# Performance work log

Measured on AMD Instinct MI355X. Metric: run time of the kernel, lower is better.

The kernel has to match this reference:

```python
import jax, jax.numpy as jnp
import numpy as np

DIMS = (2000, 500, 400)
H, DK, DV = 8, 32, 32
DM = H * DV  # 256
NUM_CLASS = 5
BS = 16384
TEMP = DK ** 0.5
LN_EPS = 1e-6


def setup_inputs() -> dict:
    key = jax.random.key(0)
    ks = jax.random.split(key, 32)
    inp = {"input_data": jax.random.normal(ks[0], (BS, sum(DIMS)), dtype=jnp.float32)}
    i = 1
    for name, odim in (("q", H * DK), ("k", H * DK), ("v", H * DV)):
        for m, d in enumerate(DIMS):
            inp[f"w{name}{m}"] = jax.random.normal(ks[i], (d, odim), dtype=jnp.float32) * (1.0 / np.sqrt(d)); i += 1
            inp[f"b{name}{m}"] = jnp.zeros((odim,), dtype=jnp.float32)
    inp["fc_w"] = jax.random.normal(ks[i], (DM, DM), dtype=jnp.float32) * (1.0 / np.sqrt(DM)); i += 1
    inp["fc_b"] = jnp.zeros((DM,), dtype=jnp.float32)
    inp["ln_g"] = jnp.ones((DM,), dtype=jnp.float32)
    inp["ln_b"] = jnp.zeros((DM,), dtype=jnp.float32)
    inp["out_w"] = jax.random.normal(ks[i], (len(DIMS) * DM, NUM_CLASS), dtype=jnp.float32) * (1.0 / np.sqrt(len(DIMS) * DM)); i += 1
    inp["out_b"] = jnp.zeros((NUM_CLASS,), dtype=jnp.float32)
    return inp


def _forward(input_data, wq, bq, wk, bk, wv, bv, fc_w, fc_b, ln_g, ln_b, out_w, out_b):
    bs = input_data.shape[0]
    M = len(DIMS)
    offs = np.concatenate([[0], np.cumsum(DIMS)])
    xs = [input_data[:, offs[m]:offs[m + 1]] for m in range(M)]
    # per-modality projections -> [bs, M, H*D]
    q = jnp.stack([xs[m] @ wq[m] + bq[m] for m in range(M)], axis=1)
    k = jnp.stack([xs[m] @ wk[m] + bk[m] for m in range(M)], axis=1)
    v = jnp.stack([xs[m] @ wv[m] + bv[m] for m in range(M)], axis=1)
    # [bs, H, M, D]
    qh = q.reshape(bs, M, H, DK).transpose(0, 2, 1, 3)
    kh = k.reshape(bs, M, H, DK).transpose(0, 2, 1, 3)
    vh = v.reshape(bs, M, H, DV).transpose(0, 2, 1, 3)
    attn = jnp.einsum("bhmd,bhnd->bhmn", qh / TEMP, kh)
    attn = attn / jnp.abs(attn.min())  # global-min scaling as in source
    attn = attn / jnp.maximum(jnp.sum(jnp.abs(attn), axis=-1, keepdims=True), 1e-12)  # L1 normalize
    attn = jax.nn.softmax(attn, axis=-1)
    o = jnp.einsum("bhmn,bhnd->bhmd", attn, vh)
    o = o.transpose(0, 2, 1, 3).reshape(bs, M, DM)
    residual = v  # [bs, M, DM]
    o = o @ fc_w + fc_b
    x = o + residual
    mu = x.mean(axis=-1, keepdims=True)
    var = ((x - mu) ** 2).mean(axis=-1, keepdims=True)
    x = (x - mu) / jnp.sqrt(var + LN_EPS) * ln_g + ln_b
    return x.reshape(bs, -1) @ out_w + out_b


def reference(input_data, wq0, bq0, wq1, bq1, wq2, bq2, wk0, bk0, wk1, bk1, wk2, bk2,
              wv0, bv0, wv1, bv1, wv2, bv2, fc_w, fc_b, ln_g, ln_b, out_w, out_b):
    return _forward(input_data, (wq0, wq1, wq2), (bq0, bq1, bq2), (wk0, wk1, wk2), (bk0, bk1, bk2),
                    (wv0, wv1, wv2), (bv0, bv1, bv2), fc_w, fc_b, ln_g, ln_b, out_w, out_b)
```

## Files before the change

### kernel.cpp

```cpp
#include <hip/hip_runtime.h>
#include <hip/hip_bf16.h>

#define BATCH 16384
#define HEADS 8
#define DDK 32
#define NQKV 768
#define NCLASS 5
#define LN_EPS 1e-6f

#define BM 128
#define BN 128
#define BKK 32

typedef _Float16 f16x8 __attribute__((ext_vector_type(8)));
typedef float f32x4 __attribute__((ext_vector_type(4)));

__device__ __forceinline__ void gl16(const void* g, void* l) {
    __builtin_amdgcn_global_load_lds(
        (const __attribute__((address_space(1))) unsigned int*)g,
        (__attribute__((address_space(3))) unsigned int*)l, 16, 0, 0);
}

__global__ __launch_bounds__(256) void convert_x(const float* __restrict__ X,
                                                 _Float16* __restrict__ A,
                                                 int Kdim, int Kpad, int xoff,
                                                 int r0, int nrows) {
    const int k8n = Kpad >> 3;
    const int total = nrows * k8n;
    for (int i = blockIdx.x * blockDim.x + threadIdx.x; i < total;
         i += gridDim.x * blockDim.x) {
        const int rl = i / k8n;
        const int k8 = (i - rl * k8n) << 3;
        const float* src = X + (size_t)(r0 + rl) * 2900 + xoff + k8;
        float xv[8];
        if (k8 + 8 <= Kdim) {
            float4 v0 = *reinterpret_cast<const float4*>(src);
            float4 v1 = *reinterpret_cast<const float4*>(src + 4);
            xv[0] = v0.x; xv[1] = v0.y; xv[2] = v0.z; xv[3] = v0.w;
            xv[4] = v1.x; xv[5] = v1.y; xv[6] = v1.z; xv[7] = v1.w;
        } else {
#pragma unroll
            for (int j = 0; j < 8; ++j) xv[j] = (k8 + j < Kdim) ? src[j] : 0.f;
        }
        union { _Float16 h[8]; uint4 v; } hi, lo;
#pragma unroll
        for (int j = 0; j < 8; ++j) {
            hi.h[j] = (_Float16)xv[j];
            lo.h[j] = (_Float16)(xv[j] - (float)hi.h[j]);
        }
        _Float16* dst = A + (size_t)rl * (2 * Kpad) + k8;
        *reinterpret_cast<uint4*>(dst) = hi.v;
        *reinterpret_cast<uint4*>(dst + Kpad) = lo.v;
    }
}

struct WArgs {
    const float* w[3][3];
    const float* b[3][3];
    const float* fcw;
    _Float16* Bt;
    float* biasx;
    _Float16* fcWh;
};

__global__ __launch_bounds__(256) void convert_w_all(WArgs a) {
    const int y = blockIdx.y;
    const int gid = blockIdx.x * 256 + threadIdx.x;
    if (y < 3) {
        const int m = y;
        const int Kdim = (m == 0) ? 2000 : (m == 1 ? 500 : 400);
        const int Kpad = (m == 0) ? 2048 : (m == 1 ? 512 : 448);
        if (gid < NQKV) {
            const int p = gid >> 8, c = gid & 255;
            a.biasx[m * NQKV + gid] = a.b[p][m][c];
        }
        const int k8n = Kpad >> 3;
        const int total = NQKV * k8n;
        _Float16* dst0 = a.Bt + (size_t)m * NQKV * 2048;
        for (int i = gid; i < total; i += gridDim.x * 256) {
            const int kb = i / NQKV;
            const int n = i - kb * NQKV;
            const int k8 = kb << 3;
            const int p = n >> 8, c = n & 255;
            const float* wsrc = a.w[p][m];
            union { _Float16 h[8]; uint4 v; } hi;
#pragma unroll
            for (int j = 0; j < 8; ++j) {
                float x = (k8 + j < Kdim) ? wsrc[(size_t)(k8 + j) * 256 + c] : 0.f;
                hi.h[j] = (_Float16)x;
            }
            *reinterpret_cast<uint4*>(dst0 + (size_t)n * Kpad + k8) = hi.v;
        }
    } else {
        for (int i = gid; i < 256 * 32; i += gridDim.x * 256) {
            const int n = i & 255;
            const int k8 = (i >> 8) << 3;
            union { _Float16 h[8]; uint4 v; } hi;
#pragma unroll
            for (int j = 0; j < 8; ++j)
                hi.h[j] = (_Float16)a.fcw[(size_t)(k8 + j) * 256 + n];
            *reinterpret_cast<uint4*>(a.fcWh + (size_t)n * 256 + k8) = hi.v;
        }
    }
}

__global__ __launch_bounds__(256) void qkv_mfma(
    const _Float16* __restrict__ A,
    const _Float16* __restrict__ Bt,
    const float* __restrict__ bias,
    float* __restrict__ Qo, float* __restrict__ Ko, float* __restrict__ Vo,
    int Kpad, int mz, int r0) {
    const int ld = 2 * Kpad;
    const int row0l = blockIdx.x * BM;
    const int nb = blockIdx.y * BN;
    const int tid = threadIdx.x;
    const int lane = tid & 63;
    const int w = tid >> 6;
    const int wr = w >> 1, wc = w & 1;

    __shared__ alignas(16) _Float16 AsH[BM * BKK];
    __shared__ alignas(16) _Float16 AsL[BM * BKK];
    __shared__ alignas(16) _Float16 BsH[BN * BKK];

    f32x4 acc[4][4];
#pragma unroll
    for (int i = 0; i < 4; ++i)
#pragma unroll
        for (int j = 0; j < 4; ++j) acc[i][j] = (f32x4){0.f, 0.f, 0.f, 0.f};

    const int rs = lane >> 2;
    const int kk = (lane & 3) * 8;
    const size_t gA0 = (size_t)(row0l + w * 16 + rs) * ld + kk;
    const size_t gA1 = (size_t)(row0l + (w + 4) * 16 + rs) * ld + kk;
    const size_t gB0 = (size_t)(nb + w * 16 + rs) * Kpad + kk;
    const size_t gB1 = (size_t)(nb + (w + 4) * 16 + rs) * Kpad + kk;
    _Float16* lAH0 = &AsH[w * 512];
    _Float16* lAH1 = &AsH[(w + 4) * 512];
    _Float16* lAL0 = &AsL[w * 512];
    _Float16* lAL1 = &AsL[(w + 4) * 512];
    _Float16* lBH0 = &BsH[w * 512];
    _Float16* lBH1 = &BsH[(w + 4) * 512];

    const int fr = lane & 15;
    const int fk = (lane >> 4) * 8;
    const int aoff0 = (wr * 64 + fr) * BKK + fk;
    const int boff0 = (wc * 64 + fr) * BKK + fk;

    const int nk = Kpad >> 5;
#pragma unroll 1
    for (int kt = 0; kt < nk; ++kt) {
        const int k0 = kt * BKK;
        __syncthreads();
        gl16(A + gA0 + k0, lAH0);
        gl16(A + gA1 + k0, lAH1);
        gl16(A + Kpad + gA0 + k0, lAL0);
        gl16(A + Kpad + gA1 + k0, lAL1);
        gl16(Bt + gB0 + k0, lBH0);
        gl16(Bt + gB1 + k0, lBH1);
        __syncthreads();

        f16x8 ah[4], bh[4];
#pragma unroll
        for (int mi = 0; mi < 4; ++mi)
            ah[mi] = *reinterpret_cast<const f16x8*>(&AsH[aoff0 + mi * 16 * BKK]);
#pragma unroll
        for (int ni = 0; ni < 4; ++ni)
            bh[ni] = *reinterpret_cast<const f16x8*>(&BsH[boff0 + ni * 16 * BKK]);
#pragma unroll
        for (int mi = 0; mi < 4; ++mi)
#pragma unroll
            for (int ni = 0; ni < 4; ++ni)
                acc[mi][ni] = __builtin_amdgcn_mfma_f32_16x16x32_f16(
                    ah[mi], bh[ni], acc[mi][ni], 0, 0, 0);
        {
            f16x8 al[4];
#pragma unroll
            for (int mi = 0; mi < 4; ++mi)
                al[mi] = *reinterpret_cast<const f16x8*>(&AsL[aoff0 + mi * 16 * BKK]);
#pragma unroll
            for (int mi = 0; mi < 4; ++mi)
#pragma unroll
                for (int ni = 0; ni < 4; ++ni)
                    acc[mi][ni] = __builtin_amdgcn_mfma_f32_16x16x32_f16(
                        al[mi], bh[ni], acc[mi][ni], 0, 0, 0);
        }
    }

#pragma unroll
    for (int ni = 0; ni < 4; ++ni) {
        const int gc = nb + wc * 64 + ni * 16 + fr;
        const int proj = gc >> 8;
        const int col = gc & 255;
        const float bv = bias[gc];
        float* outp = (proj == 0 ? Qo : proj == 1 ? Ko : Vo);
#pragma unroll
        for (int mi = 0; mi < 4; ++mi) {
            const int gr = r0 + row0l + wr * 64 + mi * 16 + (lane >> 4) * 4;
            float* p = outp + (size_t)gr * NQKV + mz * 256 + col;
#pragma unroll
            for (int j = 0; j < 4; ++j)
                p[(size_t)j * NQKV] = acc[mi][ni][j] + bv;
        }
    }
}

__global__ __launch_bounds__(256) void attn_kernel(const float* __restrict__ Q,
                                                   const float* __restrict__ K,
                                                   const float* __restrict__ V,
                                                   _Float16* __restrict__ Of) {
    const int s = blockIdx.x;
    const int t = threadIdx.x;
    __shared__ float qs[NQKV], ks[NQKV], vs[NQKV];
    __shared__ float att[HEADS][3][3];

    const size_t base = (size_t)s * NQKV;
    for (int i = t; i < NQKV; i += 256) {
        qs[i] = Q[base + i];
        ks[i] = K[base + i];
        vs[i] = V[base + i];
    }
    __syncthreads();

    if (t < 72) {
        const int h = t / 9, ij = t % 9, i = ij / 3, j = ij % 3;
        const float* qp = &qs[i * 256 + h * 32];
        const float* kp = &ks[j * 256 + h * 32];
        float sc = 0.f;
#pragma unroll
        for (int d = 0; d < DDK; ++d) sc = fmaf(qp[d], kp[d], sc);
        att[h][i][j] = sc;
    }
    __syncthreads();
    if (t < 24) {
        const int h = t / 3, i = t % 3;
        float s0 = att[h][i][0], s1 = att[h][i][1], s2 = att[h][i][2];
        float r = fabsf(s0) + fabsf(s1) + fabsf(s2);
        r = fmaxf(r, 1e-12f);
        float p0 = s0 / r, p1 = s1 / r, p2 = s2 / r;
        float mx = fmaxf(p0, fmaxf(p1, p2));
        float e0 = expf(p0 - mx), e1 = expf(p1 - mx), e2 = expf(p2 - mx);
        float inv = 1.f / (e0 + e1 + e2);
        att[h][i][0] = e0 * inv;
        att[h][i][1] = e1 * inv;
        att[h][i][2] = e2 * inv;
    }
    __syncthreads();

    const int c = t;
    const int h = c >> 5;
#pragma unroll
    for (int m = 0; m < 3; ++m) {
        float o = att[h][m][0] * vs[c] + att[h][m][1] * vs[256 + c] + att[h][m][2] * vs[512 + c];
        const size_t ob = ((size_t)s * 3 + m) * 512 + c;
        _Float16 oh = (_Float16)o;
        Of[ob] = oh;
        Of[ob + 256] = (_Float16)(o - (float)oh);
    }
}

__global__ __launch_bounds__(256) void fc_mfma(const _Float16* __restrict__ O,
                                               const _Float16* __restrict__ Wh,
                                               const float* __restrict__ fcb,
                                               const float* __restrict__ resid,
                                               float* __restrict__ X) {
    const int row0 = blockIdx.x * BM;
    const int nb = blockIdx.y * BN;
    const int tid = threadIdx.x;
    const int lane = tid & 63;
    const int w = tid >> 6;
    const int wr = w >> 1, wc = w & 1;

    __shared__ alignas(16) _Float16 AsH[BM * BKK];
    __shared__ alignas(16) _Float16 AsL[BM * BKK];
    __shared__ alignas(16) _Float16 BsH[BN * BKK];

    f32x4 acc[4][4];
#pragma unroll
    for (int i = 0; i < 4; ++i)
#pragma unroll
        for (int j = 0; j < 4; ++j) acc[i][j] = (f32x4){0.f, 0.f, 0.f, 0.f};

    const int rs = lane >> 2;
    const int kk = (lane & 3) * 8;
    const size_t gA0 = (size_t)(row0 + w * 16 + rs) * 512 + kk;
    const size_t gA1 = (size_t)(row0 + (w + 4) * 16 + rs) * 512 + kk;
    const size_t gB0 = (size_t)(nb + w * 16 + rs) * 256 + kk;
    const size_t gB1 = (size_t)(nb + (w + 4) * 16 + rs) * 256 + kk;
    _Float16* lAH0 = &AsH[w * 512];
    _Float16* lAH1 = &AsH[(w + 4) * 512];
    _Float16* lAL0 = &AsL[w * 512];
    _Float16* lAL1 = &AsL[(w + 4) * 512];
    _Float16* lBH0 = &BsH[w * 512];
    _Float16* lBH1 = &BsH[(w + 4) * 512];

    const int fr = lane & 15;
    const int fk = (lane >> 4) * 8;
    const int aoff0 = (wr * 64 + fr) * BKK + fk;
    const int boff0 = (wc * 64 + fr) * BKK + fk;

#pragma unroll 1
    for (int kt = 0; kt < 8; ++kt) {
        const int k0 = kt * BKK;
        __syncthreads();
        gl16(O + gA0 + k0, lAH0);
        gl16(O + gA1 + k0, lAH1);
        gl16(O + 256 + gA0 + k0, lAL0);
        gl16(O + 256 + gA1 + k0, lAL1);
        gl16(Wh + gB0 + k0, lBH0);
        gl16(Wh + gB1 + k0, lBH1);
        __syncthreads();

        f16x8 ah[4], bh[4];
#pragma unroll
        for (int mi = 0; mi < 4; ++mi)
            ah[mi] = *reinterpret_cast<const f16x8*>(&AsH[aoff0 + mi * 16 * BKK]);
#pragma unroll
        for (int ni = 0; ni < 4; ++ni)
            bh[ni] = *reinterpret_cast<const f16x8*>(&BsH[boff0 + ni * 16 * BKK]);
#pragma unroll
        for (int mi = 0; mi < 4; ++mi)
#pragma unroll
            for (int ni = 0; ni < 4; ++ni)
                acc[mi][ni] = __builtin_amdgcn_mfma_f32_16x16x32_f16(
                    ah[mi], bh[ni], acc[mi][ni], 0, 0, 0);
        {
            f16x8 al[4];
#pragma unroll
            for (int mi = 0; mi < 4; ++mi)
                al[mi] = *reinterpret_cast<const f16x8*>(&AsL[aoff0 + mi * 16 * BKK]);
#pragma unroll
            for (int mi = 0; mi < 4; ++mi)
#pragma unroll
                for (int ni = 0; ni < 4; ++ni)
                    acc[mi][ni] = __builtin_amdgcn_mfma_f32_16x16x32_f16(
                        al[mi], bh[ni], acc[mi][ni], 0, 0, 0);
        }
    }

#pragma unroll
    for (int ni = 0; ni < 4; ++ni) {
        const int gc = nb + wc * 64 + ni * 16 + fr;
        const float bv = fcb[gc];
#pragma unroll
        for (int mi = 0; mi < 4; ++mi) {
            const int gr = row0 + wr * 64 + mi * 16 + (lane >> 4) * 4;
#pragma unroll
            for (int j = 0; j < 4; ++j) {
                const size_t off = (size_t)(gr + j) * 256 + gc;
                X[off] = acc[mi][ni][j] + bv + resid[off];
            }
        }
    }
}

__global__ __launch_bounds__(256) void ln_out_kernel(const float* __restrict__ X,
                                                     const float* __restrict__ g,
                                                     const float* __restrict__ bb,
                                                     const float* __restrict__ ow,
                                                     const float* __restrict__ ob,
                                                     float* __restrict__ out) {
    const int s = blockIdx.x;
    const int t = threadIdx.x;
    const int lane = t & 63, wv = t >> 6;
    __shared__ float xr[NQKV];
    __shared__ float red1[4], red2[4];
    __shared__ float cpart[4][NCLASS];

    const size_t base = (size_t)s * NQKV;
    const float gg = g[t];
    const float bbv = bb[t];

    for (int m = 0; m < 3; ++m) {
        float v = X[base + m * 256 + t];
        float s1 = v, s2 = v * v;
#pragma unroll
        for (int off = 32; off > 0; off >>= 1) {
            s1 += __shfl_down(s1, off);
            s2 += __shfl_down(s2, off);
        }
        if (lane == 0) { red1[wv] = s1; red2[wv] = s2; }
        __syncthreads();
        const float tot = red1[0] + red1[1] + red1[2] + red1[3];
        const float tot2 = red2[0] + red2[1] + red2[2] + red2[3];
        const float mu = tot * (1.f / 256.f);
        const float var = tot2 * (1.f / 256.f) - mu * mu;
        const float inv = 1.0f / sqrtf(var + LN_EPS);
        xr[m * 256 + t] = (v - mu) * inv * gg + bbv;
        __syncthreads();
    }

    float p[NCLASS] = {0.f, 0.f, 0.f, 0.f, 0.f};
    for (int i = t; i < NQKV; i += 256) {
        const float xv = xr[i];
#pragma unroll
        for (int c = 0; c < NCLASS; ++c) p[c] = fmaf(xv, ow[i * NCLASS + c], p[c]);
    }
#pragma unroll
    for (int c = 0; c < NCLASS; ++c) {
        float pv = p[c];
#pragma unroll
        for (int off = 32; off > 0; off >>= 1) pv += __shfl_down(pv, off);
        if (lane == 0) cpart[wv][c] = pv;
    }
    __syncthreads();
    if (t < NCLASS)
        out[(size_t)s * NCLASS + t] =
            cpart[0][t] + cpart[1][t] + cpart[2][t] + cpart[3][t] + ob[t];
}

extern "C" void kernel_launch(void* const* d_in, const int* in_sizes, int n_in,
                              void* d_out, int out_size, void* d_ws, size_t ws_size,
                              hipStream_t stream) {
    const float* x = (const float*)d_in[0];
    WArgs wa;
    int idx = 1;
    for (int p = 0; p < 3; ++p)
        for (int m = 0; m < 3; ++m) {
            wa.w[p][m] = (const float*)d_in[idx++];
            wa.b[p][m] = (const float*)d_in[idx++];
        }
    const float* fc_w = (const float*)d_in[19];
    const float* fc_b = (const float*)d_in[20];
    const float* ln_g = (const float*)d_in[21];
    const float* ln_b = (const float*)d_in[22];
    const float* out_w = (const float*)d_in[23];
    const float* out_b = (const float*)d_in[24];

    float* ws = (float*)d_ws;
    const size_t SZ = (size_t)BATCH * NQKV;
    float* Q = ws;
    float* Kb = ws + SZ;
    float* Vb = ws + 2 * SZ;
    float* biasx = ws + 3 * SZ;
    _Float16* Bt = (_Float16*)(biasx + 3 * NQKV);
    _Float16* fcWh = Bt + (size_t)3 * NQKV * 2048;
    _Float16* pool = fcWh + 256 * 256;

    wa.fcw = fc_w; wa.Bt = Bt; wa.biasx = biasx; wa.fcWh = fcWh;

    const size_t fixed_bytes = (size_t)((char*)pool - (char*)d_ws);
    const size_t avail = (ws_size > fixed_bytes) ? ws_size - fixed_bytes : 0;

    float* X = Q;
    _Float16* Of = pool;

    const int Kdim[3] = {2000, 500, 400};
    const int Kpad[3] = {2048, 512, 448};
    const int xoff[3] = {0, 2000, 2500};

    convert_w_all<<<dim3(768, 4), 256, 0, stream>>>(wa);

    for (int m = 0; m < 3; ++m) {
        size_t rc = (avail / ((size_t)4 * Kpad[m])) & ~(size_t)127;
        if (rc < 128) rc = 128;
        if (rc > BATCH) rc = BATCH;
        const int rows_chunk = (int)rc;
        for (int r0 = 0; r0 < BATCH; r0 += rows_chunk) {
            const int nr = (BATCH - r0 < rows_chunk) ? (BATCH - r0) : rows_chunk;
            const int cgrid = ((nr * (Kpad[m] >> 3)) + 255) / 256;
            convert_x<<<(cgrid < 2048 ? cgrid : 2048), 256, 0, stream>>>(
                x, pool, Kdim[m], Kpad[m], xoff[m], r0, nr);
            dim3 g(nr / BM, NQKV / BN);
            qkv_mfma<<<g, 256, 0, stream>>>(pool, Bt + (size_t)m * NQKV * 2048,
                                            biasx + m * NQKV, Q, Kb, Vb,
                                            Kpad[m], m, r0);
        }
    }

    attn_kernel<<<BATCH, 256, 0, stream>>>(Q, Kb, Vb, Of);

    fc_mfma<<<dim3((BATCH * 3) / BM, 2), 256, 0, stream>>>(Of, fcWh, fc_b, Vb, X);

    ln_out_kernel<<<BATCH, 256, 0, stream>>>(X, ln_g, ln_b, out_w, out_b, (float*)d_out);
}
```

Baseline: 733.7 us.

## Merge per-modality QKV GEMMs into one launch with concatenated hi/lo K

```diff
diff --git a/kernel.cpp b/kernel.cpp
--- a/kernel.cpp
+++ b/kernel.cpp
@@ -21,16 +21,28 @@
         (__attribute__((address_space(3))) unsigned int*)l, 16, 0, 0);
 }
 
-__global__ __launch_bounds__(256) void convert_x(const float* __restrict__ X,
-                                                 _Float16* __restrict__ A,
-                                                 int Kdim, int Kpad, int xoff,
-                                                 int r0, int nrows) {
-    const int k8n = Kpad >> 3;
-    const int total = nrows * k8n;
+__global__ __launch_bounds__(256) void convert_x_all(const float* __restrict__ X,
+                                                     _Float16* __restrict__ A0,
+                                                     _Float16* __restrict__ A1,
+                                                     _Float16* __restrict__ A2,
+                                                     int r0, int nrows) {
+    const int total = nrows * 384;
     for (int i = blockIdx.x * blockDim.x + threadIdx.x; i < total;
          i += gridDim.x * blockDim.x) {
-        const int rl = i / k8n;
-        const int k8 = (i - rl * k8n) << 3;
+        const int rl = i / 384;
+        const int slot = i - rl * 384;
+        int k8, Kdim, xoff, lo_off;
+        _Float16* dst;
+        if (slot < 256) {
+            k8 = slot << 3; Kdim = 2000; xoff = 0; lo_off = 2048;
+            dst = A0 + (size_t)rl * 4096 + k8;
+        } else if (slot < 320) {
+            k8 = (slot - 256) << 3; Kdim = 500; xoff = 2000; lo_off = 512;
+            dst = A1 + (size_t)rl * 1024 + k8;
+        } else {
+            k8 = (slot - 320) << 3; Kdim = 400; xoff = 2500; lo_off = 512;
+            dst = A2 + (size_t)rl * 1024 + k8;
+        }
         const float* src = X + (size_t)(r0 + rl) * 2900 + xoff + k8;
         float xv[8];
         if (k8 + 8 <= Kdim) {
@@ -48,9 +60,8 @@
             hi.h[j] = (_Float16)xv[j];
             lo.h[j] = (_Float16)(xv[j] - (float)hi.h[j]);
         }
-        _Float16* dst = A + (size_t)rl * (2 * Kpad) + k8;
         *reinterpret_cast<uint4*>(dst) = hi.v;
-        *reinterpret_cast<uint4*>(dst + Kpad) = lo.v;
+        *reinterpret_cast<uint4*>(dst + lo_off) = lo.v;
     }
 }
 
@@ -69,14 +80,17 @@
     if (y < 3) {
         const int m = y;
         const int Kdim = (m == 0) ? 2000 : (m == 1 ? 500 : 400);
-        const int Kpad = (m == 0) ? 2048 : (m == 1 ? 512 : 448);
+        const int Kpad = (m == 0) ? 2048 : 512;
         if (gid < NQKV) {
             const int p = gid >> 8, c = gid & 255;
             a.biasx[m * NQKV + gid] = a.b[p][m][c];
         }
+        _Float16* dst0 = a.Bt;
+        if (m >= 1) dst0 += (size_t)NQKV * 4096;
+        if (m == 2) dst0 += (size_t)NQKV * 1024;
+        const int ld = 2 * Kpad;
         const int k8n = Kpad >> 3;
         const int total = NQKV * k8n;
-        _Float16* dst0 = a.Bt + (size_t)m * NQKV * 2048;
         for (int i = gid; i < total; i += gridDim.x * 256) {
             const int kb = i / NQKV;
             const int n = i - kb * NQKV;
@@ -89,7 +103,8 @@
                 float x = (k8 + j < Kdim) ? wsrc[(size_t)(k8 + j) * 256 + c] : 0.f;
                 hi.h[j] = (_Float16)x;
             }
-            *reinterpret_cast<uint4*>(dst0 + (size_t)n * Kpad + k8) = hi.v;
+            *reinterpret_cast<uint4*>(dst0 + (size_t)n * ld + k8) = hi.v;
+            *reinterpret_cast<uint4*>(dst0 + (size_t)n * ld + Kpad + k8) = hi.v;
         }
     } else {
         for (int i = gid; i < 256 * 32; i += gridDim.x * 256) {
@@ -104,13 +119,23 @@
     }
 }
 
-__global__ __launch_bounds__(256) void qkv_mfma(
-    const _Float16* __restrict__ A,
-    const _Float16* __restrict__ Bt,
-    const float* __restrict__ bias,
+struct GemmArgs {
+    const _Float16* A[3];
+    const _Float16* B[3];
+    int keff[3];
+};
+
+__global__ __launch_bounds__(256) void qkv_mfma_all(
+    GemmArgs ga, const float* __restrict__ biasx,
     float* __restrict__ Qo, float* __restrict__ Ko, float* __restrict__ Vo,
-    int Kpad, int mz, int r0) {
-    const int ld = 2 * Kpad;
+    int r0) {
+    const int z = blockIdx.z;
+    const _Float16* __restrict__ A = ga.A[z];
+    const _Float16* __restrict__ Bt = ga.B[z];
+    const int ld = ga.keff[z];
+    const int nk = ld >> 5;
+    const float* __restrict__ bias = biasx + z * NQKV;
+
     const int row0l = blockIdx.x * BM;
     const int nb = blockIdx.y * BN;
     const int tid = threadIdx.x;
@@ -118,9 +143,8 @@
     const int w = tid >> 6;
     const int wr = w >> 1, wc = w & 1;
 
-    __shared__ alignas(16) _Float16 AsH[BM * BKK];
-    __shared__ alignas(16) _Float16 AsL[BM * BKK];
-    __shared__ alignas(16) _Float16 BsH[BN * BKK];
+    __shared__ alignas(16) _Float16 As[BM * BKK];
+    __shared__ alignas(16) _Float16 Bs[BN * BKK];
 
     f32x4 acc[4][4];
 #pragma unroll
@@ -131,59 +155,42 @@
     const int rs = lane >> 2;
     const int kk = (lane & 3) * 8;
     const size_t gA0 = (size_t)(row0l + w * 16 + rs) * ld + kk;
-    const size_t gA1 = (size_t)(row0l + (w + 4) * 16 + rs) * ld + kk;
-    const size_t gB0 = (size_t)(nb + w * 16 + rs) * Kpad + kk;
-    const size_t gB1 = (size_t)(nb + (w + 4) * 16 + rs) * Kpad + kk;
-    _Float16* lAH0 = &AsH[w * 512];
-    _Float16* lAH1 = &AsH[(w + 4) * 512];
-    _Float16* lAL0 = &AsL[w * 512];
-    _Float16* lAL1 = &AsL[(w + 4) * 512];
-    _Float16* lBH0 = &BsH[w * 512];
-    _Float16* lBH1 = &BsH[(w + 4) * 512];
+    const size_t gA1 = gA0 + (size_t)64 * ld;
+    const size_t gB0 = (size_t)(nb + w * 16 + rs) * ld + kk;
+    const size_t gB1 = gB0 + (size_t)64 * ld;
+    _Float16* lA0 = &As[(w * 16) * BKK];
+    _Float16* lA1 = &As[(64 + w * 16) * BKK];
+    _Float16* lB0 = &Bs[(w * 16) * BKK];
+    _Float16* lB1 = &Bs[(64 + w * 16) * BKK];
 
     const int fr = lane & 15;
     const int fk = (lane >> 4) * 8;
     const int aoff0 = (wr * 64 + fr) * BKK + fk;
     const int boff0 = (wc * 64 + fr) * BKK + fk;
 
-    const int nk = Kpad >> 5;
 #pragma unroll 1
     for (int kt = 0; kt < nk; ++kt) {
         const int k0 = kt * BKK;
         __syncthreads();
-        gl16(A + gA0 + k0, lAH0);
-        gl16(A + gA1 + k0, lAH1);
-        gl16(A + Kpad + gA0 + k0, lAL0);
-        gl16(A + Kpad + gA1 + k0, lAL1);
-        gl16(Bt + gB0 + k0, lBH0);
-        gl16(Bt + gB1 + k0, lBH1);
-        __syncthreads();
-
-        f16x8 ah[4], bh[4];
+        gl16(A + gA0 + k0, lA0);
+        gl16(A + gA1 + k0, lA1);
+        gl16(Bt + gB0 + k0, lB0);
+        gl16(Bt + gB1 + k0, lB1);
+        __syncthreads();
+
+        f16x8 a[4], b[4];
 #pragma unroll
         for (int mi = 0; mi < 4; ++mi)
-            ah[mi] = *reinterpret_cast<const f16x8*>(&AsH[aoff0 + mi * 16 * BKK]);
+            a[mi] = *reinterpret_cast<const f16x8*>(&As[aoff0 + mi * 16 * BKK]);
 #pragma unroll
         for (int ni = 0; ni < 4; ++ni)
-            bh[ni] = *reinterpret_cast<const f16x8*>(&BsH[boff0 + ni * 16 * BKK]);
+            b[ni] = *reinterpret_cast<const f16x8*>(&Bs[boff0 + ni * 16 * BKK]);
 #pragma unroll
         for (int mi = 0; mi < 4; ++mi)
 #pragma unroll
             for (int ni = 0; ni < 4; ++ni)
                 acc[mi][ni] = __builtin_amdgcn_mfma_f32_16x16x32_f16(
-                    ah[mi], bh[ni], acc[mi][ni], 0, 0, 0);
-        {
-            f16x8 al[4];
-#pragma unroll
-            for (int mi = 0; mi < 4; ++mi)
-                al[mi] = *reinterpret_cast<const f16x8*>(&AsL[aoff0 + mi * 16 * BKK]);
-#pragma unroll
-            for (int mi = 0; mi < 4; ++mi)
-#pragma unroll
-                for (int ni = 0; ni < 4; ++ni)
-                    acc[mi][ni] = __builtin_amdgcn_mfma_f32_16x16x32_f16(
-                        al[mi], bh[ni], acc[mi][ni], 0, 0, 0);
-        }
+                    a[mi], b[ni], acc[mi][ni], 0, 0, 0);
     }
 
 #pragma unroll
@@ -196,7 +203,7 @@
 #pragma unroll
         for (int mi = 0; mi < 4; ++mi) {
             const int gr = r0 + row0l + wr * 64 + mi * 16 + (lane >> 4) * 4;
-            float* p = outp + (size_t)gr * NQKV + mz * 256 + col;
+            float* p = outp + (size_t)gr * NQKV + z * 256 + col;
 #pragma unroll
             for (int j = 0; j < 4; ++j)
                 p[(size_t)j * NQKV] = acc[mi][ni][j] + bv;
@@ -433,38 +440,41 @@
     float* Vb = ws + 2 * SZ;
     float* biasx = ws + 3 * SZ;
     _Float16* Bt = (_Float16*)(biasx + 3 * NQKV);
-    _Float16* fcWh = Bt + (size_t)3 * NQKV * 2048;
+    _Float16* fcWh = Bt + (size_t)NQKV * 6144;
     _Float16* pool = fcWh + 256 * 256;
 
     wa.fcw = fc_w; wa.Bt = Bt; wa.biasx = biasx; wa.fcWh = fcWh;
 
     const size_t fixed_bytes = (size_t)((char*)pool - (char*)d_ws);
     const size_t avail = (ws_size > fixed_bytes) ? ws_size - fixed_bytes : 0;
+    size_t rc = (avail / 12288) & ~(size_t)127;
+    if (rc < 128) rc = 128;
+    if (rc > BATCH) rc = BATCH;
+    const int rows_chunk = (int)rc;
 
     float* X = Q;
     _Float16* Of = pool;
 
-    const int Kdim[3] = {2000, 500, 400};
-    const int Kpad[3] = {2048, 512, 448};
-    const int xoff[3] = {0, 2000, 2500};
-
     convert_w_all<<<dim3(768, 4), 256, 0, stream>>>(wa);
 
-    for (int m = 0; m < 3; ++m) {
-        size_t rc = (avail / ((size_t)4 * Kpad[m])) & ~(size_t)127;
-        if (rc < 128) rc = 128;
-        if (rc > BATCH) rc = BATCH;
-        const int rows_chunk = (int)rc;
-        for (int r0 = 0; r0 < BATCH; r0 += rows_chunk) {
-            const int nr = (BATCH - r0 < rows_chunk) ? (BATCH - r0) : rows_chunk;
-            const int cgrid = ((nr * (Kpad[m] >> 3)) + 255) / 256;
-            convert_x<<<(cgrid < 2048 ? cgrid : 2048), 256, 0, stream>>>(
-                x, pool, Kdim[m], Kpad[m], xoff[m], r0, nr);
-            dim3 g(nr / BM, NQKV / BN);
-            qkv_mfma<<<g, 256, 0, stream>>>(pool, Bt + (size_t)m * NQKV * 2048,
-                                            biasx + m * NQKV, Q, Kb, Vb,
-                                            Kpad[m], m, r0);
-        }
+    GemmArgs ga;
+    ga.keff[0] = 4096; ga.keff[1] = 1024; ga.keff[2] = 1024;
+    ga.B[0] = Bt;
+    ga.B[1] = Bt + (size_t)NQKV * 4096;
+    ga.B[2] = Bt + (size_t)NQKV * 5120;
+
+    _Float16* A0 = pool;
+    _Float16* A1 = A0 + (size_t)rows_chunk * 4096;
+    _Float16* A2 = A1 + (size_t)rows_chunk * 1024;
+    ga.A[0] = A0; ga.A[1] = A1; ga.A[2] = A2;
+
+    for (int r0 = 0; r0 < BATCH; r0 += rows_chunk) {
+        const int nr = (BATCH - r0 < rows_chunk) ? (BATCH - r0) : rows_chunk;
+        const int cgrid = (nr * 384 + 255) / 256;
+        convert_x_all<<<(cgrid < 2048 ? cgrid : 2048), 256, 0, stream>>>(
+            x, A0, A1, A2, r0, nr);
+        dim3 g(nr / BM, NQKV / BN, 3);
+        qkv_mfma_all<<<g, 256, 0, stream>>>(ga, biasx, Q, Kb, Vb, r0);
     }
 
     attn_kernel<<<BATCH, 256, 0, stream>>>(Q, Kb, Vb, Of);
```

After: 706.5 us. 3.7% less time.
